# Optimization experiments

Measured on AMD Instinct MI355X. Metric: run time of the kernel, lower is better.

Reference implementation:

```python
import jax, jax.numpy as jnp
import numpy as np

D_MODEL = 2048
N_HEADS = 16
N_KV = 4
D_HEAD = D_MODEL // N_HEADS  # 128
N_REP = N_HEADS // N_KV      # 4
ROPE_BASE = 1000000.0


def _rope_tables(T, d_head, dtype):
    # inv_freq = (1/base)^(2i/d) for i in [0, d/2)
    i = jnp.arange(d_head // 2, dtype=jnp.float32)
    inv_freq = (1.0 / ROPE_BASE) ** (2.0 * i / d_head)
    theta = jnp.arange(T, dtype=jnp.float32)[:, None] * inv_freq[None, :]  # [T, d/2]
    theta = jnp.concatenate([theta, theta], axis=-1)                        # [T, d]
    return jnp.sin(theta).astype(dtype), jnp.cos(theta).astype(dtype)


def _apply_rope(x, sin, cos):
    # x: [B, h, T, d]; sin/cos: [T, d]
    x1, x2 = jnp.split(x, 2, axis=-1)
    rot = jnp.concatenate([-x2, x1], axis=-1)
    return cos[None, None] * x + sin[None, None] * rot


def setup_inputs() -> dict:
    key = jax.random.key(0)
    ks = jax.random.split(key, 9)
    B, T = 2, 2048
    s_in = 1.0 / np.sqrt(D_MODEL)
    return {
        "x": jax.random.normal(ks[0], (B, T, D_MODEL), jnp.float32),
        "wq": jax.random.normal(ks[1], (D_MODEL, N_HEADS * D_HEAD), jnp.float32) * s_in,
        "bq": jax.random.normal(ks[2], (N_HEADS * D_HEAD,), jnp.float32) * 0.02,
        "wk": jax.random.normal(ks[3], (D_MODEL, N_KV * D_HEAD), jnp.float32) * s_in,
        "bk": jax.random.normal(ks[4], (N_KV * D_HEAD,), jnp.float32) * 0.02,
        "wv": jax.random.normal(ks[5], (D_MODEL, N_KV * D_HEAD), jnp.float32) * s_in,
        "bv": jax.random.normal(ks[6], (N_KV * D_HEAD,), jnp.float32) * 0.02,
        "wo": jax.random.normal(ks[7], (D_MODEL, D_MODEL), jnp.float32) * s_in,
    }


def reference(x, wq, bq, wk, bk, wv, bv, wo):
    B, T, C = x.shape
    sin, cos = _rope_tables(T, D_HEAD, x.dtype)

    q = (x @ wq + bq).reshape(B, T, N_HEADS, D_HEAD).transpose(0, 2, 1, 3)  # [B,H,T,d]
    k = (x @ wk + bk).reshape(B, T, N_KV, D_HEAD).transpose(0, 2, 1, 3)     # [B,KV,T,d]
    v = (x @ wv + bv).reshape(B, T, N_KV, D_HEAD).transpose(0, 2, 1, 3)     # [B,KV,T,d]

    q = _apply_rope(q, sin, cos)
    k = _apply_rope(k, sin, cos)

    # GQA: group query heads as [B, KV, rep, T, d] to broadcast against k/v
    qg = q.reshape(B, N_KV, N_REP, T, D_HEAD)
    scale = 1.0 / jnp.sqrt(jnp.asarray(D_HEAD, x.dtype))
    scores = jnp.einsum('bkrqd,bksd->bkrqs', qg, k) * scale  # [B,KV,rep,T,S]

    causal = jnp.tril(jnp.ones((T, T), dtype=bool))
    neg = jnp.asarray(jnp.finfo(x.dtype).min, x.dtype)
    scores = jnp.where(causal[None, None, None], scores, neg)
    p = jax.nn.softmax(scores, axis=-1)

    out = jnp.einsum('bkrqs,bksd->bkrqd', p, v)               # [B,KV,rep,T,d]
    out = out.reshape(B, N_HEADS, T, D_HEAD).transpose(0, 2, 1, 3).reshape(B, T, C)
    return out @ wo, k, v
```

## Files before the change

kernel.cpp:

```cpp
#include <hip/hip_runtime.h>
#include <hip/hip_bf16.h>
#include <math.h>

#define BB 2
#define TT 2048
#define DMODEL 2048
#define NH 16
#define NKV 4
#define DH 128
#define NQKV 3072
#define MM (BB*TT)

typedef unsigned short u16;
typedef unsigned int u32;

typedef __bf16 bf16x8 __attribute__((ext_vector_type(8)));
typedef __bf16 bf16x4 __attribute__((ext_vector_type(4)));
typedef short short4v __attribute__((ext_vector_type(4)));
typedef float f32x4 __attribute__((ext_vector_type(4)));

__device__ __forceinline__ u16 f2b(float f) {
  union { float f; u32 u; } v; v.f = f;
  u32 r = v.u + 0x7fffu + ((v.u >> 16) & 1u);
  return (u16)(r >> 16);
}
__device__ __forceinline__ float b2f(u16 h) {
  union { u32 u; float f; } v; v.u = ((u32)h) << 16;
  return v.f;
}
__device__ __forceinline__ u32 pack2bf(float x, float y) {
  union { float f; u32 u; } a, b; a.f = x; b.f = y;
  return ((a.u + 0x8000u) >> 16) | ((b.u + 0x8000u) & 0xffff0000u);
}

__device__ __forceinline__ void gload16(const void* g, void* l) {
  __builtin_amdgcn_global_load_lds(
      (const __attribute__((address_space(1))) unsigned int*)g,
      (__attribute__((address_space(3))) unsigned int*)l, 16, 0, 0);
}

__device__ __forceinline__ float fast_exp2(float x) {
#if __has_builtin(__builtin_amdgcn_exp2f)
  return __builtin_amdgcn_exp2f(x);
#else
  return __expf(x * 0.6931471805599453f);
#endif
}

__device__ __forceinline__ f32x4 mfma16(bf16x4 a, bf16x4 b, f32x4 c) {
#if __has_builtin(__builtin_amdgcn_mfma_f32_16x16x16bf16_1k)
  union { bf16x4 b; short4v s; } ua, ub;
  ua.b = a; ub.b = b;
  return __builtin_amdgcn_mfma_f32_16x16x16bf16_1k(ua.s, ub.s, c, 0, 0, 0);
#elif __has_builtin(__builtin_amdgcn_mfma_f32_16x16x16_bf16)
  return __builtin_amdgcn_mfma_f32_16x16x16_bf16(a, b, c, 0, 0, 0);
#else
  asm volatile("v_mfma_f32_16x16x16_bf16 %0, %1, %2, %0"
               : "+v"(c) : "v"(a), "v"(b));
  return c;
#endif
}

__global__ void cvt_x_kernel(const float* __restrict__ x, u16* __restrict__ xb, int n4) {
  int i = blockIdx.x * 256 + threadIdx.x;
  if (i < n4) {
    float4 v = ((const float4*)x)[i];
    u32 lo = (u32)f2b(v.x) | ((u32)f2b(v.y) << 16);
    u32 hi = (u32)f2b(v.z) | ((u32)f2b(v.w) << 16);
    uint2 r; r.x = lo; r.y = hi;
    ((uint2*)xb)[i] = r;
  }
}

__global__ void rope_table_kernel(float2* __restrict__ tab) {
  int i = blockIdx.x * 256 + threadIdx.x;
  int t = i >> 6, d = i & 63;
  float inv = exp2f(-(float)d * 0.31143075889569023f);
  float th = (float)t * inv;
  float2 cs; cs.x = cosf(th); cs.y = sinf(th);
  tab[i] = cs;
}

__global__ void transpose_cvt_kernel(const float* __restrict__ src, u16* __restrict__ dst,
                                     int srcCols, int dstRowOff) {
  __shared__ u16 t[64][65];
  int c0 = blockIdx.x * 64, r0 = blockIdx.y * 64;
  int tid = threadIdx.x;
  for (int i = tid; i < 4096; i += 256) {
    int r = i >> 6, c = i & 63;
    t[r][c] = f2b(src[(size_t)(r0 + r) * srcCols + c0 + c]);
  }
  __syncthreads();
  for (int i = tid; i < 4096; i += 256) {
    int n = i >> 6, k = i & 63;
    dst[(size_t)(dstRowOff + c0 + n) * 2048 + r0 + k] = t[k][n];
  }
}


#define BARRIER asm volatile("s_barrier" ::: "memory")
#define LGKM0   asm volatile("s_waitcnt lgkmcnt(0)" ::: "memory")

#define STAGE_A(H, KT, RB) do { \
    const u16* g_ = gA + (size_t)(H) * 262144 + (size_t)(KT) * 64; \
    gload16(g_,          sm + (RB) + tid * 8); \
    gload16(g_ + 131072, sm + (RB) + 4096 + tid * 8); \
  } while (0)

#define STAGE_B(H, KT, RB) do { \
    const u16* g_ = gB + (size_t)(H) * 262144 + (size_t)(KT) * 64; \
    gload16(g_,          sm + (RB) + tid * 8); \
    gload16(g_ + 131072, sm + (RB) + 4096 + tid * 8); \
  } while (0)

#define LDA(BU, MH) do { \
    const u16* ab_ = sm + (BU) + (MH) * 8192 + lra * 64; \
    _Pragma("unroll") \
    for (int mi = 0; mi < 4; mi++) { \
      a[mi][0] = *(const bf16x8*)&ab_[mi * 1024 + as0]; \
      a[mi][1] = *(const bf16x8*)&ab_[mi * 1024 + as1]; \
    } \
  } while (0)

#define LDB(BU, NL) do { \
    const u16* bb_ = sm + (BU) + 16384 + hb * 8192 + lrb * 64; \
    _Pragma("unroll") \
    for (int nj = 0; nj < 2; nj++) { \
      b[(NL)*2+nj][0] = *(const bf16x8*)&bb_[((NL)*2+nj) * 1024 + bs0]; \
      b[(NL)*2+nj][1] = *(const bf16x8*)&bb_[((NL)*2+nj) * 1024 + bs1]; \
    } \
  } while (0)

#define MFMAQ(MH, NL) do { \
    _Pragma("unroll") \
    for (int mi = 0; mi < 4; mi++) \
      _Pragma("unroll") \
      for (int nj = 0; nj < 2; nj++) { \
        acc[(MH)*4+mi][(NL)*2+nj] = __builtin_amdgcn_mfma_f32_16x16x32_bf16( \
            a[mi][0], b[(NL)*2+nj][0], acc[(MH)*4+mi][(NL)*2+nj], 0, 0, 0); \
        acc[(MH)*4+mi][(NL)*2+nj] = __builtin_amdgcn_mfma_f32_16x16x32_bf16( \
            a[mi][1], b[(NL)*2+nj][1], acc[(MH)*4+mi][(NL)*2+nj], 0, 0, 0); \
      } \
  } while (0)

#define TILE4(BU, OBU, KA1, KN) do { \
     \
    LDA(BU, 0); LDB(BU, 0); \
    STAGE_A(1, KA1, (OBU) + 8192); \
    BARRIER; LGKM0; \
    __builtin_amdgcn_s_setprio(1); MFMAQ(0, 0); __builtin_amdgcn_s_setprio(0); \
    BARRIER; \
     \
    LDB(BU, 1); \
    STAGE_A(0, KN, (BU)); \
    BARRIER; LGKM0; \
    __builtin_amdgcn_s_setprio(1); MFMAQ(0, 1); __builtin_amdgcn_s_setprio(0); \
    BARRIER; \
     \
    LDA(BU, 1); \
    STAGE_B(0, KN, (BU) + 16384); \
    BARRIER; LGKM0; \
    __builtin_amdgcn_s_setprio(1); MFMAQ(1, 1); __builtin_amdgcn_s_setprio(0); \
    BARRIER; \
     \
    STAGE_B(1, KN, (BU) + 24576); \
    BARRIER; LGKM0; \
    __builtin_amdgcn_s_setprio(1); MFMAQ(1, 0); __builtin_amdgcn_s_setprio(0); \
    asm volatile("s_waitcnt vmcnt(6)\n\ts_barrier" ::: "memory"); \
  } while (0)

__global__ __launch_bounds__(512, 2) void gemm_qkv_kernel(
    const u16* __restrict__ A, const u16* __restrict__ Bt,
    const float* __restrict__ bq, const float* __restrict__ bk,
    const float* __restrict__ bv, const float2* __restrict__ rtab,
    u16* __restrict__ qb, u16* __restrict__ kb, u16* __restrict__ vt,
    float* __restrict__ outK, float* __restrict__ outV) {
  __shared__ __align__(16) u16 sm[65536];
  const int tid  = threadIdx.x;
  const int lane = tid & 63;
  const int wave = tid >> 6;
  const int wm   = wave >> 2;
  const int wn   = wave & 3;
  const int quad = lane >> 4;
  const int l16  = lane & 15;
  const int m0 = blockIdx.y * 256;
  const int n0 = blockIdx.x * 256;
  const int bx = blockIdx.x;

  const int srow = tid >> 3;
  const int sch  = (tid & 7) ^ (srow & 7);
  const u16* gA = A  + (size_t)(m0 + srow) * 2048 + sch * 8;
  const u16* gB = Bt + (size_t)(n0 + srow) * 2048 + sch * 8;

  const int lra = wm * 64 + l16;
  const int lrb = (wn & 1) * 64 + l16;
  const int hb  = wn >> 1;
  const int as0 = ((quad)     ^ (lra & 7)) << 3;
  const int as1 = ((quad + 4) ^ (lra & 7)) << 3;
  const int bs0 = ((quad)     ^ (lrb & 7)) << 3;
  const int bs1 = ((quad + 4) ^ (lrb & 7)) << 3;

  bf16x8 a[4][2], b[4][2];
  f32x4 acc[8][4];
  const f32x4 zero = {0.f, 0.f, 0.f, 0.f};
#pragma unroll
  for (int i = 0; i < 8; i++)
#pragma unroll
    for (int j = 0; j < 4; j++) acc[i][j] = zero;

  STAGE_A(0, 0, 0);
  STAGE_B(0, 0, 16384);
  STAGE_B(1, 0, 24576);
  STAGE_A(1, 0, 8192);
  STAGE_A(0, 1, 32768);
  STAGE_B(0, 1, 32768 + 16384);
  STAGE_B(1, 1, 32768 + 24576);
  asm volatile("s_waitcnt vmcnt(6)\n\ts_barrier" ::: "memory");

#pragma unroll 1
  for (int it2 = 0; it2 < 16; ++it2) {
    const int ka1 = (2 * it2 + 1) & 31;
    const int kn0 = (2 * it2 + 2) & 31;
    const int kn1 = (2 * it2 + 3) & 31;
    TILE4(0,     32768, ka1, kn0);
    TILE4(32768, 0,     kn0, kn1);
  }

  asm volatile("s_waitcnt vmcnt(0)\n\ts_barrier" ::: "memory");

  const int cls = (bx < 8) ? 0 : ((bx < 10) ? 1 : 2);
#pragma unroll
  for (int nf = 0; nf < 4; nf++) {
    int col = wn * 64 + nf * 16 + l16;
    int gcol = n0 + col;
    float bval = (cls == 0) ? bq[gcol] : ((cls == 1) ? bk[gcol - 2048] : bv[gcol - 2560]);
#pragma unroll
    for (int mh = 0; mh < 2; mh++)
#pragma unroll
      for (int mi = 0; mi < 4; mi++)
#pragma unroll
        for (int r = 0; r < 4; r++) {
          int row = mh * 128 + wm * 64 + mi * 16 + quad * 4 + r;
          int ci = (row * 256 + col) ^ ((row & 7) << 3);
          sm[ci] = f2b(acc[mh * 4 + mi][nf][r] + bval);
        }
  }
  __syncthreads();

  const int bidx = m0 >> 11;
  const int trow0 = m0 & 2047;

  if (cls < 2) {
    const int isQ = (cls == 0);
#pragma unroll
    for (int itq = 0; itq < 8; itq++) {
      int id = tid + itq * 512;
      int lh = id >> 11;
      int rem = id & 2047;
      int row = rem >> 3, oc = rem & 7;
      int t = trow0 + row;
      int rl = t & 63, ttile = t >> 6;
      int sw = (row & 7) << 3;
      int i0 = (row * 256 + lh * 128 + oc * 8);
      uint4 lo = *(const uint4*)&sm[i0 ^ sw];
      uint4 hi = *(const uint4*)&sm[(i0 + 64) ^ sw];
      const u16* plo = (const u16*)&lo;
      const u16* phi = (const u16*)&hi;
      u16 y1[8], y2[8];
      float f1[8], f2v[8];
#pragma unroll
      for (int j = 0; j < 8; j++) {
        float2 cs = rtab[(t << 6) + oc * 8 + j];
        float x1 = b2f(plo[j]), x2 = b2f(phi[j]);
        f1[j]  = cs.x * x1 - cs.y * x2;
        f2v[j] = cs.x * x2 + cs.y * x1;
        y1[j] = f2b(f1[j]);
        y2[j] = f2b(f2v[j]);
      }
      if (isQ) {
        int hh = bx * 2 + lh;
        size_t tb = ((size_t)(bidx * NH + hh) * 32 + ttile) * 8192;
        *(uint4*)&qb[tb + (size_t)((oc)     * 64 + rl) * 8] = *(const uint4*)y1;
        *(uint4*)&qb[tb + (size_t)((oc + 8) * 64 + rl) * 8] = *(const uint4*)y2;
      } else {
        int hh = bx * 2 + lh - 16;
        size_t tb = ((size_t)(bidx * NKV + hh) * 32 + ttile) * 8192;
        *(uint4*)&kb[tb + (size_t)((oc)     * 64 + rl) * 8] = *(const uint4*)y1;
        *(uint4*)&kb[tb + (size_t)((oc + 8) * 64 + rl) * 8] = *(const uint4*)y2;
        size_t base = ((size_t)(bidx * NKV + hh) * TT + t) * DH + oc * 8;
        *(float4*)&outK[base]          = *(const float4*)&f1[0];
        *(float4*)&outK[base + 4]      = *(const float4*)&f1[4];
        *(float4*)&outK[base + 64]     = *(const float4*)&f2v[0];
        *(float4*)&outK[base + 64 + 4] = *(const float4*)&f2v[4];
      }
    }
  } else {
#pragma unroll
    for (int itv = 0; itv < 16; itv++) {
      int id = tid + itv * 512;
      int lh = id >> 12;
      int rem = id & 4095;
      int row = rem >> 4, oc = rem & 15;
      int kvh = bx * 2 + lh - 20;
      int i0 = (row * 256 + lh * 128 + oc * 8) ^ ((row & 7) << 3);
      uint4 v = *(const uint4*)&sm[i0];
      const u16* pv = (const u16*)&v;
      float f[8];
#pragma unroll
      for (int j = 0; j < 8; j++) f[j] = b2f(pv[j]);
      size_t base = ((size_t)(bidx * NKV + kvh) * TT + trow0 + row) * DH + oc * 8;
      *(float4*)&outV[base]     = *(const float4*)&f[0];
      *(float4*)&outV[base + 4] = *(const float4*)&f[4];
    }
#pragma unroll
    for (int itv = 0; itv < 16; itv++) {
      int id = tid + itv * 512;
      int lh = id >> 12;
      int rem = id & 4095;
      int st = rem >> 10;
      int rem2 = rem & 1023;
      int chunk = rem2 >> 7, dl = rem2 & 127;
      int m = chunk >> 2, qd = chunk & 3;
      int kvh = bx * 2 + lh - 20;
      u16 tmp[8];
#pragma unroll
      for (int e = 0; e < 8; e++) {
        int srw = (2 * m + (e >> 2)) * 16 + qd * 4 + (e & 3);
        int row = st * 64 + srw;
        int idx = (row * 256 + lh * 128 + dl) ^ ((row & 7) << 3);
        tmp[e] = sm[idx];
      }
      int tt = (trow0 >> 6) + st;
      size_t tilebase = ((size_t)(bidx * NKV + kvh) * 32 + tt) * 8192;
      *(uint4*)&vt[tilebase + (size_t)(chunk * 128 + dl) * 8] = *(const uint4*)tmp;
    }
  }
}

__global__ __launch_bounds__(256, 3) void gemm_out_kernel(
    const u16* __restrict__ A, const u16* __restrict__ Bt,
    float* __restrict__ Cout, int M, int N, int K) {
  __shared__ __align__(16) u16 smo[16384];
  const int tid  = threadIdx.x;
  const int lane = tid & 63;
  const int wave = tid >> 6;
  const int quad = lane >> 4;
  const int l16  = lane & 15;
  const int m0 = blockIdx.y * 128;
  const int n0 = blockIdx.x * 128;
  const int wrow = (wave >> 1) * 64;
  const int wcol = (wave & 1) * 64;

  f32x4 acc[4][4];
  const f32x4 zero = {0.f, 0.f, 0.f, 0.f};
#pragma unroll
  for (int i = 0; i < 4; i++)
#pragma unroll
    for (int j = 0; j < 4; j++) acc[i][j] = zero;

  const int srow = tid >> 2;
  const int scol = (tid & 3) * 8;
  const u16* ga = A  + (size_t)(m0 + srow) * K + scol;
  const u16* gb = Bt + (size_t)(n0 + srow) * K + scol;

  gload16(ga,                  &smo[tid * 8]);
  gload16(ga + (size_t)64 * K, &smo[2048 + tid * 8]);
  gload16(gb,                  &smo[4096 + tid * 8]);
  gload16(gb + (size_t)64 * K, &smo[6144 + tid * 8]);

  for (int k0 = 0; k0 < K; k0 += 32) {
    const int p = (k0 >> 5) & 1;
    const int kn = (k0 + 32 == K) ? 0 : k0 + 32;
    u16* nb = &smo[(p ^ 1) * 8192];
    gload16(ga + kn,                  nb + tid * 8);
    gload16(ga + kn + (size_t)64 * K, nb + 2048 + tid * 8);
    gload16(gb + kn,                  nb + 4096 + tid * 8);
    gload16(gb + kn + (size_t)64 * K, nb + 6144 + tid * 8);
    asm volatile("s_waitcnt vmcnt(4)\n\ts_barrier" ::: "memory");
    const u16* cb = &smo[p * 8192];
    bf16x8 af[4], bf[4];
#pragma unroll
    for (int mi = 0; mi < 4; mi++)
      af[mi] = *(const bf16x8*)&cb[(wrow + mi * 16 + l16) * 32 + quad * 8];
#pragma unroll
    for (int ni = 0; ni < 4; ni++)
      bf[ni] = *(const bf16x8*)&cb[4096 + (wcol + ni * 16 + l16) * 32 + quad * 8];
    asm volatile("s_waitcnt lgkmcnt(0)\n\ts_barrier" ::: "memory");
#pragma unroll
    for (int mi = 0; mi < 4; mi++)
#pragma unroll
      for (int ni = 0; ni < 4; ni++)
        acc[mi][ni] = __builtin_amdgcn_mfma_f32_16x16x32_bf16(af[mi], bf[ni], acc[mi][ni], 0, 0, 0);
  }
  asm volatile("s_waitcnt vmcnt(0)" ::: "memory");

#pragma unroll
  for (int ni = 0; ni < 4; ni++) {
    int gcol = n0 + wcol + ni * 16 + l16;
#pragma unroll
    for (int mi = 0; mi < 4; mi++) {
#pragma unroll
      for (int r = 0; r < 4; r++) {
        int grow = m0 + wrow + mi * 16 + quad * 4 + r;
        Cout[(size_t)grow * N + gcol] = acc[mi][ni][r];
      }
    }
  }
}

__global__ __launch_bounds__(256, 2) void attn_kernel(
    const u16* __restrict__ Qt, const u16* __restrict__ Kt,
    const u16* __restrict__ Vt, u16* __restrict__ Ob) {
  __shared__ __align__(16) u16 sm[24576];
  u16* vbuf = sm + 16384;

  const int bh = blockIdx.y;
  const int b = bh >> 4, h = bh & 15, kv = h >> 2;
  const int tid = threadIdx.x;
  const int lane = tid & 63;
  const int wave = tid >> 6;
  const int quad = lane >> 4;
  const int l16 = lane & 15;

  const u16* qbase = Qt + (size_t)(b * NH + h) * 32 * 8192;
  const u16* kbase = Kt + (size_t)(b * NKV + kv) * 32 * 8192;
  const u16* vbase = Vt + (size_t)(b * NKV + kv) * 32 * 8192;

  const f32x4 zero = {0.f, 0.f, 0.f, 0.f};
  const float SC2 = 0.08838834764831845f * 1.4426950408889634f;
  const float NEGINF = -__builtin_inff();

  int par = 0;

#pragma unroll
  for (int p = 0; p < 4; p++)
    gload16(kbase + p * 2048 + tid * 8, sm + p * 2048 + tid * 8);

  for (int half = 0; half < 2; ++half) {
    const int qt = half ? (31 - (int)blockIdx.x) : (int)blockIdx.x;
    const int q0 = qt * 64;
    const u16* qtile = qbase + (size_t)qt * 8192;
    const int qrel = wave * 16 + l16;

    bf16x8 qf[4];
#pragma unroll
    for (int kc = 0; kc < 4; kc++)
      qf[kc] = *(const bf16x8*)&qtile[(size_t)((kc * 4 + quad) * 64 + qrel) * 8];

    float mrow = NEGINF, lrow = 0.f;
    f32x4 o[8];
#pragma unroll
    for (int d = 0; d < 8; d++) o[d] = zero;

    for (int kt = 0; kt <= qt; ++kt) {
      u16* kb_c = sm + par * 8192;
      u16* kb_n = sm + (par ^ 1) * 8192;
      const int ktn = (kt < qt) ? kt + 1 : 0;
      const u16* vsrc = vbase + (size_t)kt * 8192;
      const u16* knxt = kbase + (size_t)ktn * 8192;
#pragma unroll
      for (int p = 0; p < 4; p++)
        gload16(vsrc + p * 2048 + tid * 8, vbuf + p * 2048 + tid * 8);
#pragma unroll
      for (int p = 0; p < 4; p++)
        gload16(knxt + p * 2048 + tid * 8, kb_n + p * 2048 + tid * 8);
      asm volatile("s_waitcnt vmcnt(8)\n\ts_barrier" ::: "memory");

      f32x4 sv[4];
#pragma unroll
      for (int mt = 0; mt < 4; mt++) sv[mt] = zero;
#pragma unroll
      for (int kc = 0; kc < 4; kc++) {
#pragma unroll
        for (int mt = 0; mt < 4; mt++) {
          bf16x8 kf = *(const bf16x8*)&kb_c[(size_t)((kc * 4 + quad) * 64 + mt * 16 + l16) * 8];
          sv[mt] = __builtin_amdgcn_mfma_f32_16x16x32_bf16(kf, qf[kc], sv[mt], 0, 0, 0);
        }
      }

      if (kt == qt) {
#pragma unroll
        for (int mt = 0; mt < 4; mt++)
#pragma unroll
          for (int r = 0; r < 4; r++) {
            int srel = mt * 16 + quad * 4 + r;
            if (srel > qrel) sv[mt][r] = NEGINF;
          }
      }
      float mraw = NEGINF;
#pragma unroll
      for (int mt = 0; mt < 4; mt++)
#pragma unroll
        for (int r = 0; r < 4; r++) mraw = fmaxf(mraw, sv[mt][r]);
      mraw = fmaxf(mraw, __shfl_xor(mraw, 16));
      mraw = fmaxf(mraw, __shfl_xor(mraw, 32));

      float mnew = fmaxf(mrow, mraw);
      float alpha = fast_exp2((mrow - mnew) * SC2);
      mrow = mnew;
      float msc = mnew * SC2;
      float lsum = 0.f;
#pragma unroll
      for (int mt = 0; mt < 4; mt++) {
#pragma unroll
        for (int r = 0; r < 4; r++) {
          float p = fast_exp2(__builtin_fmaf(sv[mt][r], SC2, -msc));
          sv[mt][r] = p;
          lsum += p;
        }
      }
      lrow = lrow * alpha + lsum;
      bf16x4 pb[4];
#pragma unroll
      for (int mt = 0; mt < 4; mt++) {
        union { u32 u[2]; bf16x4 v; } pu;
        pu.u[0] = pack2bf(sv[mt][0], sv[mt][1]);
        pu.u[1] = pack2bf(sv[mt][2], sv[mt][3]);
        pb[mt] = pu.v;
      }
#pragma unroll
      for (int dt = 0; dt < 8; dt++) {
        o[dt][0] *= alpha; o[dt][1] *= alpha; o[dt][2] *= alpha; o[dt][3] *= alpha;
      }

      asm volatile("s_waitcnt vmcnt(4)\n\ts_barrier" ::: "memory");
#pragma unroll
      for (int m = 0; m < 2; m++) {
#pragma unroll
        for (int dt = 0; dt < 8; dt++) {
          bf16x8 vf = *(const bf16x8*)&vbuf[(size_t)(((m * 4 + quad) * 128) + dt * 16 + l16) * 8];
          bf16x4 vlo = __builtin_shufflevector(vf, vf, 0, 1, 2, 3);
          bf16x4 vhi = __builtin_shufflevector(vf, vf, 4, 5, 6, 7);
          o[dt] = mfma16(vlo, pb[2 * m],     o[dt]);
          o[dt] = mfma16(vhi, pb[2 * m + 1], o[dt]);
        }
      }
      asm volatile("s_barrier" ::: "memory");
      par ^= 1;
    }

    lrow += __shfl_xor(lrow, 16);
    lrow += __shfl_xor(lrow, 32);
    float inv = 1.0f / lrow;
    int t = q0 + qrel;
    size_t rowbase = (size_t)(b * TT + t) * DMODEL + h * DH;
#pragma unroll
    for (int dt = 0; dt < 8; dt++) {
      uint2 w;
      w.x = pack2bf(o[dt][0] * inv, o[dt][1] * inv);
      w.y = pack2bf(o[dt][2] * inv, o[dt][3] * inv);
      *(uint2*)&Ob[rowbase + dt * 16 + quad * 4] = w;
    }
  }
  asm volatile("s_waitcnt vmcnt(0)" ::: "memory");
}

extern "C" void kernel_launch(void* const* d_in, const int* in_sizes, int n_in,
                              void* d_out, int out_size, void* d_ws, size_t ws_size,
                              hipStream_t stream) {
  (void)in_sizes; (void)n_in; (void)out_size; (void)ws_size;
  const float* x  = (const float*)d_in[0];
  const float* wq = (const float*)d_in[1];
  const float* bq = (const float*)d_in[2];
  const float* wk = (const float*)d_in[3];
  const float* bk = (const float*)d_in[4];
  const float* wv = (const float*)d_in[5];
  const float* bv = (const float*)d_in[6];
  const float* wo = (const float*)d_in[7];
  float* out = (float*)d_out;

  char* ws = (char*)d_ws;
  u16*    xb    = (u16*)(ws);
  u16*    wqkvT = (u16*)(ws + 16777216);
  u16*    woT   = (u16*)(ws + 29360128);
  float2* rtab  = (float2*)(ws + 37748736);
  u16*    qb    = (u16*)(ws + 38797312);
  u16*    kb    = (u16*)(ws + 55574528);
  u16*    vt    = (u16*)(ws + 59768832);
  u16*    ob    = (u16*)(ws + 63963136);

  float* outK = out + (size_t)BB * TT * DMODEL;
  float* outV = outK + (size_t)BB * NKV * TT * DH;

  cvt_x_kernel<<<8192, 256, 0, stream>>>(x, xb, (BB * TT * DMODEL) / 4);
  rope_table_kernel<<<512, 256, 0, stream>>>(rtab);
  transpose_cvt_kernel<<<dim3(32, 32), 256, 0, stream>>>(wq, wqkvT, 2048, 0);
  transpose_cvt_kernel<<<dim3(8, 32),  256, 0, stream>>>(wk, wqkvT, 512, 2048);
  transpose_cvt_kernel<<<dim3(8, 32),  256, 0, stream>>>(wv, wqkvT, 512, 2560);
  transpose_cvt_kernel<<<dim3(32, 32), 256, 0, stream>>>(wo, woT, 2048, 0);

  gemm_qkv_kernel<<<dim3(NQKV / 256, MM / 256), 512, 0, stream>>>(
      xb, wqkvT, bq, bk, bv, rtab, qb, kb, vt, outK, outV);

  attn_kernel<<<dim3(16, BB * NH), 256, 0, stream>>>(qb, kb, vt, ob);

  gemm_out_kernel<<<dim3(DMODEL / 128, MM / 128), 256, 0, stream>>>(
      ob, woT, out, MM, DMODEL, DMODEL);
}
```

Measured before the change: 303.3 us.

## Process paired causal query tiles together in attention; merge weight transposes

The attention kernel now processes both query tiles of a causal pair (p and 31-p) in one pass over K/V. It streams each K/V tile once and reuses it for both tiles, instead of running two sequential passes that each reload K/V. It also adds lazy softmax rescaling, which skips the alpha rescale when the new row max exceeds the old one by no more than a threshold, and adds MFMA priority hints. The four weight transpose launches are fused into one launch, and extra lgkmcnt waits are inserted in the QKV GEMM pipeline. Holding two sets of accumulators raises register pressure.

```diff
diff --git a/kernel.cpp b/kernel.cpp
--- a/kernel.cpp
+++ b/kernel.cpp
@@ -81,10 +81,20 @@
   tab[i] = cs;
 }
 
-__global__ void transpose_cvt_kernel(const float* __restrict__ src, u16* __restrict__ dst,
-                                     int srcCols, int dstRowOff) {
+__global__ void transpose_cvt_all_kernel(const float* __restrict__ wq,
+                                         const float* __restrict__ wk,
+                                         const float* __restrict__ wv,
+                                         const float* __restrict__ wo,
+                                         u16* __restrict__ wqkvT,
+                                         u16* __restrict__ woT) {
   __shared__ u16 t[64][65];
-  int c0 = blockIdx.x * 64, r0 = blockIdx.y * 64;
+  int bx = blockIdx.x;
+  const float* src; u16* dst; int srcCols, rowOff, cb;
+  if (bx < 32)      { src = wq; dst = wqkvT; srcCols = 2048; rowOff = 0;    cb = bx; }
+  else if (bx < 40) { src = wk; dst = wqkvT; srcCols = 512;  rowOff = 2048; cb = bx - 32; }
+  else if (bx < 48) { src = wv; dst = wqkvT; srcCols = 512;  rowOff = 2560; cb = bx - 40; }
+  else              { src = wo; dst = woT;   srcCols = 2048; rowOff = 0;    cb = bx - 48; }
+  int c0 = cb * 64, r0 = blockIdx.y * 64;
   int tid = threadIdx.x;
   for (int i = tid; i < 4096; i += 256) {
     int r = i >> 6, c = i & 63;
@@ -93,7 +103,7 @@
   __syncthreads();
   for (int i = tid; i < 4096; i += 256) {
     int n = i >> 6, k = i & 63;
-    dst[(size_t)(dstRowOff + c0 + n) * 2048 + r0 + k] = t[k][n];
+    dst[(size_t)(rowOff + c0 + n) * 2048 + r0 + k] = t[k][n];
   }
 }
 
@@ -147,6 +157,7 @@
      \
     LDA(BU, 0); LDB(BU, 0); \
     STAGE_A(1, KA1, (OBU) + 8192); \
+    asm volatile("s_waitcnt lgkmcnt(8)" ::: "memory"); \
     BARRIER; LGKM0; \
     __builtin_amdgcn_s_setprio(1); MFMAQ(0, 0); __builtin_amdgcn_s_setprio(0); \
     BARRIER; \
@@ -159,6 +170,7 @@
      \
     LDA(BU, 1); \
     STAGE_B(0, KN, (BU) + 16384); \
+    asm volatile("s_waitcnt lgkmcnt(4)" ::: "memory"); \
     BARRIER; LGKM0; \
     __builtin_amdgcn_s_setprio(1); MFMAQ(1, 1); __builtin_amdgcn_s_setprio(0); \
     BARRIER; \
@@ -408,6 +420,58 @@
   }
 }
 
+
+#define SM_STRIP(sv, mrow, lrow, pb, o, qt_) do { \
+    if (kt == (qt_)) { \
+      _Pragma("unroll") \
+      for (int mt = 0; mt < 4; mt++) { \
+        _Pragma("unroll") \
+        for (int r = 0; r < 4; r++) { \
+          int srel = mt * 16 + quad * 4 + r; \
+          if (srel > qrel) sv[mt][r] = NEGINF; \
+        } \
+      } \
+    } \
+    float mraw = NEGINF; \
+    _Pragma("unroll") \
+    for (int mt = 0; mt < 4; mt++) { \
+      _Pragma("unroll") \
+      for (int r = 0; r < 4; r++) mraw = fmaxf(mraw, sv[mt][r]); \
+    } \
+    mraw = fmaxf(mraw, __shfl_xor(mraw, 16)); \
+    mraw = fmaxf(mraw, __shfl_xor(mraw, 32)); \
+    bool noresc = __all(mraw <= mrow + 8.0f);    \
+    float mnew = noresc ? mrow : fmaxf(mrow, mraw); \
+    float msc = mnew * SC2; \
+    float lsum = 0.f; \
+    _Pragma("unroll") \
+    for (int mt = 0; mt < 4; mt++) { \
+      _Pragma("unroll") \
+      for (int r = 0; r < 4; r++) { \
+        float pe = fast_exp2(__builtin_fmaf(sv[mt][r], SC2, -msc)); \
+        sv[mt][r] = pe; lsum += pe; \
+      } \
+    } \
+    if (noresc) { \
+      lrow += lsum; \
+    } else { \
+      float alpha = fast_exp2((mrow - mnew) * SC2); \
+      mrow = mnew; \
+      lrow = lrow * alpha + lsum; \
+      _Pragma("unroll") \
+      for (int dt = 0; dt < 8; dt++) { \
+        o[dt][0] *= alpha; o[dt][1] *= alpha; o[dt][2] *= alpha; o[dt][3] *= alpha; \
+      } \
+    } \
+    _Pragma("unroll") \
+    for (int mt = 0; mt < 4; mt++) { \
+      union { u32 u[2]; bf16x4 v; } pu_; \
+      pu_.u[0] = pack2bf(sv[mt][0], sv[mt][1]); \
+      pu_.u[1] = pack2bf(sv[mt][2], sv[mt][3]); \
+      pb[mt] = pu_.v; \
+    } \
+  } while (0)
+
 __global__ __launch_bounds__(256, 2) void attn_kernel(
     const u16* __restrict__ Qt, const u16* __restrict__ Kt,
     const u16* __restrict__ Vt, u16* __restrict__ Ob) {
@@ -430,100 +494,80 @@
   const float SC2 = 0.08838834764831845f * 1.4426950408889634f;
   const float NEGINF = -__builtin_inff();
 
+  const int p = (bh & 16) ? (15 - (int)blockIdx.x) : (int)blockIdx.x;
+  const int qtA = p, qtB = 31 - p;
+  const int qrel = wave * 16 + l16;
+
   int par = 0;
-
-#pragma unroll
-  for (int p = 0; p < 4; p++)
-    gload16(kbase + p * 2048 + tid * 8, sm + p * 2048 + tid * 8);
-
-  for (int half = 0; half < 2; ++half) {
-    const int qt = half ? (31 - (int)blockIdx.x) : (int)blockIdx.x;
-    const int q0 = qt * 64;
-    const u16* qtile = qbase + (size_t)qt * 8192;
-    const int qrel = wave * 16 + l16;
-
-    bf16x8 qf[4];
-#pragma unroll
-    for (int kc = 0; kc < 4; kc++)
-      qf[kc] = *(const bf16x8*)&qtile[(size_t)((kc * 4 + quad) * 64 + qrel) * 8];
-
-    float mrow = NEGINF, lrow = 0.f;
-    f32x4 o[8];
-#pragma unroll
-    for (int d = 0; d < 8; d++) o[d] = zero;
-
-    for (int kt = 0; kt <= qt; ++kt) {
-      u16* kb_c = sm + par * 8192;
-      u16* kb_n = sm + (par ^ 1) * 8192;
-      const int ktn = (kt < qt) ? kt + 1 : 0;
-      const u16* vsrc = vbase + (size_t)kt * 8192;
-      const u16* knxt = kbase + (size_t)ktn * 8192;
-#pragma unroll
-      for (int p = 0; p < 4; p++)
-        gload16(vsrc + p * 2048 + tid * 8, vbuf + p * 2048 + tid * 8);
-#pragma unroll
-      for (int p = 0; p < 4; p++)
-        gload16(knxt + p * 2048 + tid * 8, kb_n + p * 2048 + tid * 8);
-      asm volatile("s_waitcnt vmcnt(8)\n\ts_barrier" ::: "memory");
-
-      f32x4 sv[4];
-#pragma unroll
-      for (int mt = 0; mt < 4; mt++) sv[mt] = zero;
+#pragma unroll
+  for (int pp = 0; pp < 4; pp++)
+    gload16(kbase + pp * 2048 + tid * 8, sm + pp * 2048 + tid * 8);
+
+  const u16* qpA = qbase + (size_t)qtA * 8192;
+  const u16* qpB = qbase + (size_t)qtB * 8192;
+  bf16x8 qfA[4], qfB[4];
+#pragma unroll
+  for (int kc = 0; kc < 4; kc++) {
+    qfA[kc] = *(const bf16x8*)&qpA[(size_t)((kc * 4 + quad) * 64 + qrel) * 8];
+    qfB[kc] = *(const bf16x8*)&qpB[(size_t)((kc * 4 + quad) * 64 + qrel) * 8];
+  }
+
+  float mA = NEGINF, lA = 0.f, mB = NEGINF, lB = 0.f;
+  f32x4 oA[8], oB[8];
+#pragma unroll
+  for (int d = 0; d < 8; d++) { oA[d] = zero; oB[d] = zero; }
+
+  for (int kt = 0; kt <= qtB; ++kt) {
+    u16* kb_c = sm + par * 8192;
+    u16* kb_n = sm + (par ^ 1) * 8192;
+    const int ktn = (kt < qtB) ? kt + 1 : 0;
+    const u16* vsrc = vbase + (size_t)kt * 8192;
+    const u16* knxt = kbase + (size_t)ktn * 8192;
+#pragma unroll
+    for (int pp = 0; pp < 4; pp++)
+      gload16(vsrc + pp * 2048 + tid * 8, vbuf + pp * 2048 + tid * 8);
+#pragma unroll
+    for (int pp = 0; pp < 4; pp++)
+      gload16(knxt + pp * 2048 + tid * 8, kb_n + pp * 2048 + tid * 8);
+    asm volatile("s_waitcnt vmcnt(8)\n\ts_barrier" ::: "memory");
+
+    const bool actA = (kt <= qtA);
+    f32x4 svA[4], svB[4];
+#pragma unroll
+    for (int mt = 0; mt < 4; mt++) { svA[mt] = zero; svB[mt] = zero; }
+
+    if (actA) {
+      __builtin_amdgcn_s_setprio(1);
 #pragma unroll
       for (int kc = 0; kc < 4; kc++) {
 #pragma unroll
         for (int mt = 0; mt < 4; mt++) {
           bf16x8 kf = *(const bf16x8*)&kb_c[(size_t)((kc * 4 + quad) * 64 + mt * 16 + l16) * 8];
-          sv[mt] = __builtin_amdgcn_mfma_f32_16x16x32_bf16(kf, qf[kc], sv[mt], 0, 0, 0);
+          svB[mt] = __builtin_amdgcn_mfma_f32_16x16x32_bf16(kf, qfB[kc], svB[mt], 0, 0, 0);
+          svA[mt] = __builtin_amdgcn_mfma_f32_16x16x32_bf16(kf, qfA[kc], svA[mt], 0, 0, 0);
         }
       }
-
-      if (kt == qt) {
-#pragma unroll
-        for (int mt = 0; mt < 4; mt++)
-#pragma unroll
-          for (int r = 0; r < 4; r++) {
-            int srel = mt * 16 + quad * 4 + r;
-            if (srel > qrel) sv[mt][r] = NEGINF;
-          }
-      }
-      float mraw = NEGINF;
-#pragma unroll
-      for (int mt = 0; mt < 4; mt++)
-#pragma unroll
-        for (int r = 0; r < 4; r++) mraw = fmaxf(mraw, sv[mt][r]);
-      mraw = fmaxf(mraw, __shfl_xor(mraw, 16));
-      mraw = fmaxf(mraw, __shfl_xor(mraw, 32));
-
-      float mnew = fmaxf(mrow, mraw);
-      float alpha = fast_exp2((mrow - mnew) * SC2);
-      mrow = mnew;
-      float msc = mnew * SC2;
-      float lsum = 0.f;
-#pragma unroll
-      for (int mt = 0; mt < 4; mt++) {
-#pragma unroll
-        for (int r = 0; r < 4; r++) {
-          float p = fast_exp2(__builtin_fmaf(sv[mt][r], SC2, -msc));
-          sv[mt][r] = p;
-          lsum += p;
+      __builtin_amdgcn_s_setprio(0);
+    } else {
+      __builtin_amdgcn_s_setprio(1);
+#pragma unroll
+      for (int kc = 0; kc < 4; kc++) {
+#pragma unroll
+        for (int mt = 0; mt < 4; mt++) {
+          bf16x8 kf = *(const bf16x8*)&kb_c[(size_t)((kc * 4 + quad) * 64 + mt * 16 + l16) * 8];
+          svB[mt] = __builtin_amdgcn_mfma_f32_16x16x32_bf16(kf, qfB[kc], svB[mt], 0, 0, 0);
         }
       }
-      lrow = lrow * alpha + lsum;
-      bf16x4 pb[4];
-#pragma unroll
-      for (int mt = 0; mt < 4; mt++) {
-        union { u32 u[2]; bf16x4 v; } pu;
-        pu.u[0] = pack2bf(sv[mt][0], sv[mt][1]);
-        pu.u[1] = pack2bf(sv[mt][2], sv[mt][3]);
-        pb[mt] = pu.v;
-      }
-#pragma unroll
-      for (int dt = 0; dt < 8; dt++) {
-        o[dt][0] *= alpha; o[dt][1] *= alpha; o[dt][2] *= alpha; o[dt][3] *= alpha;
-      }
-
-      asm volatile("s_waitcnt vmcnt(4)\n\ts_barrier" ::: "memory");
+      __builtin_amdgcn_s_setprio(0);
+    }
+
+    bf16x4 pbA[4], pbB[4];
+    SM_STRIP(svB, mB, lB, pbB, oB, qtB);
+    if (actA) SM_STRIP(svA, mA, lA, pbA, oA, qtA);
+
+    asm volatile("s_waitcnt vmcnt(4)\n\ts_barrier" ::: "memory");
+    if (actA) {
+      __builtin_amdgcn_s_setprio(1);
 #pragma unroll
       for (int m = 0; m < 2; m++) {
 #pragma unroll
@@ -531,24 +575,57 @@
           bf16x8 vf = *(const bf16x8*)&vbuf[(size_t)(((m * 4 + quad) * 128) + dt * 16 + l16) * 8];
           bf16x4 vlo = __builtin_shufflevector(vf, vf, 0, 1, 2, 3);
           bf16x4 vhi = __builtin_shufflevector(vf, vf, 4, 5, 6, 7);
-          o[dt] = mfma16(vlo, pb[2 * m],     o[dt]);
-          o[dt] = mfma16(vhi, pb[2 * m + 1], o[dt]);
+          oB[dt] = mfma16(vlo, pbB[2 * m],     oB[dt]);
+          oB[dt] = mfma16(vhi, pbB[2 * m + 1], oB[dt]);
+          oA[dt] = mfma16(vlo, pbA[2 * m],     oA[dt]);
+          oA[dt] = mfma16(vhi, pbA[2 * m + 1], oA[dt]);
         }
       }
-      asm volatile("s_barrier" ::: "memory");
-      par ^= 1;
-    }
-
-    lrow += __shfl_xor(lrow, 16);
-    lrow += __shfl_xor(lrow, 32);
-    float inv = 1.0f / lrow;
-    int t = q0 + qrel;
+      __builtin_amdgcn_s_setprio(0);
+    } else {
+      __builtin_amdgcn_s_setprio(1);
+#pragma unroll
+      for (int m = 0; m < 2; m++) {
+#pragma unroll
+        for (int dt = 0; dt < 8; dt++) {
+          bf16x8 vf = *(const bf16x8*)&vbuf[(size_t)(((m * 4 + quad) * 128) + dt * 16 + l16) * 8];
+          bf16x4 vlo = __builtin_shufflevector(vf, vf, 0, 1, 2, 3);
+          bf16x4 vhi = __builtin_shufflevector(vf, vf, 4, 5, 6, 7);
+          oB[dt] = mfma16(vlo, pbB[2 * m],     oB[dt]);
+          oB[dt] = mfma16(vhi, pbB[2 * m + 1], oB[dt]);
+        }
+      }
+      __builtin_amdgcn_s_setprio(0);
+    }
+    asm volatile("s_barrier" ::: "memory");
+    par ^= 1;
+  }
+
+  {
+    lA += __shfl_xor(lA, 16);
+    lA += __shfl_xor(lA, 32);
+    float inv = 1.0f / lA;
+    int t = qtA * 64 + qrel;
     size_t rowbase = (size_t)(b * TT + t) * DMODEL + h * DH;
 #pragma unroll
     for (int dt = 0; dt < 8; dt++) {
       uint2 w;
-      w.x = pack2bf(o[dt][0] * inv, o[dt][1] * inv);
-      w.y = pack2bf(o[dt][2] * inv, o[dt][3] * inv);
+      w.x = pack2bf(oA[dt][0] * inv, oA[dt][1] * inv);
+      w.y = pack2bf(oA[dt][2] * inv, oA[dt][3] * inv);
+      *(uint2*)&Ob[rowbase + dt * 16 + quad * 4] = w;
+    }
+  }
+  {
+    lB += __shfl_xor(lB, 16);
+    lB += __shfl_xor(lB, 32);
+    float inv = 1.0f / lB;
+    int t = qtB * 64 + qrel;
+    size_t rowbase = (size_t)(b * TT + t) * DMODEL + h * DH;
+#pragma unroll
+    for (int dt = 0; dt < 8; dt++) {
+      uint2 w;
+      w.x = pack2bf(oB[dt][0] * inv, oB[dt][1] * inv);
+      w.y = pack2bf(oB[dt][2] * inv, oB[dt][3] * inv);
       *(uint2*)&Ob[rowbase + dt * 16 + quad * 4] = w;
     }
   }
@@ -584,10 +661,7 @@
 
   cvt_x_kernel<<<8192, 256, 0, stream>>>(x, xb, (BB * TT * DMODEL) / 4);
   rope_table_kernel<<<512, 256, 0, stream>>>(rtab);
-  transpose_cvt_kernel<<<dim3(32, 32), 256, 0, stream>>>(wq, wqkvT, 2048, 0);
-  transpose_cvt_kernel<<<dim3(8, 32),  256, 0, stream>>>(wk, wqkvT, 512, 2048);
-  transpose_cvt_kernel<<<dim3(8, 32),  256, 0, stream>>>(wv, wqkvT, 512, 2560);
-  transpose_cvt_kernel<<<dim3(32, 32), 256, 0, stream>>>(wo, woT, 2048, 0);
+  transpose_cvt_all_kernel<<<dim3(80, 32), 256, 0, stream>>>(wq, wk, wv, wo, wqkvT, woT);
 
   gemm_qkv_kernel<<<dim3(NQKV / 256, MM / 256), 512, 0, stream>>>(
       xb, wqkvT, bq, bk, bv, rtab, qb, kb, vt, outK, outV);
```

Result: no change. 307.0 us (+1.2%).

## Merge weight transposes, split attention blocks per tile, add lazy softmax rescale

Applied to the files above, without the earlier changes.

The four weight transpose launches are merged into a single kernel launch that picks its source tensor from the block index. The attention kernel now gives each q-tile its own block (32 per head, interleaved so short and long tiles alternate) instead of pairing two tiles per block. It also skips the online-softmax rescale unless the new max exceeds the old by more than a threshold, and raises wave priority around the MFMA sections. The QKV GEMM gains partial lgkmcnt waits before its barriers. The threshold-based lazy rescale keeps exact normalization but lets unnormalized exponents grow, up to about 2^(8*scale), which is a small overflow and precision risk.

```diff
diff --git a/kernel.cpp b/kernel.cpp
--- a/kernel.cpp
+++ b/kernel.cpp
@@ -81,10 +81,20 @@
   tab[i] = cs;
 }
 
-__global__ void transpose_cvt_kernel(const float* __restrict__ src, u16* __restrict__ dst,
-                                     int srcCols, int dstRowOff) {
+__global__ void transpose_cvt_all_kernel(const float* __restrict__ wq,
+                                         const float* __restrict__ wk,
+                                         const float* __restrict__ wv,
+                                         const float* __restrict__ wo,
+                                         u16* __restrict__ wqkvT,
+                                         u16* __restrict__ woT) {
   __shared__ u16 t[64][65];
-  int c0 = blockIdx.x * 64, r0 = blockIdx.y * 64;
+  int bx = blockIdx.x;
+  const float* src; u16* dst; int srcCols, rowOff, cb;
+  if (bx < 32)      { src = wq; dst = wqkvT; srcCols = 2048; rowOff = 0;    cb = bx; }
+  else if (bx < 40) { src = wk; dst = wqkvT; srcCols = 512;  rowOff = 2048; cb = bx - 32; }
+  else if (bx < 48) { src = wv; dst = wqkvT; srcCols = 512;  rowOff = 2560; cb = bx - 40; }
+  else              { src = wo; dst = woT;   srcCols = 2048; rowOff = 0;    cb = bx - 48; }
+  int c0 = cb * 64, r0 = blockIdx.y * 64;
   int tid = threadIdx.x;
   for (int i = tid; i < 4096; i += 256) {
     int r = i >> 6, c = i & 63;
@@ -93,7 +103,7 @@
   __syncthreads();
   for (int i = tid; i < 4096; i += 256) {
     int n = i >> 6, k = i & 63;
-    dst[(size_t)(dstRowOff + c0 + n) * 2048 + r0 + k] = t[k][n];
+    dst[(size_t)(rowOff + c0 + n) * 2048 + r0 + k] = t[k][n];
   }
 }
 
@@ -147,6 +157,7 @@
      \
     LDA(BU, 0); LDB(BU, 0); \
     STAGE_A(1, KA1, (OBU) + 8192); \
+    asm volatile("s_waitcnt lgkmcnt(8)" ::: "memory"); \
     BARRIER; LGKM0; \
     __builtin_amdgcn_s_setprio(1); MFMAQ(0, 0); __builtin_amdgcn_s_setprio(0); \
     BARRIER; \
@@ -159,6 +170,7 @@
      \
     LDA(BU, 1); \
     STAGE_B(0, KN, (BU) + 16384); \
+    asm volatile("s_waitcnt lgkmcnt(4)" ::: "memory"); \
     BARRIER; LGKM0; \
     __builtin_amdgcn_s_setprio(1); MFMAQ(1, 1); __builtin_amdgcn_s_setprio(0); \
     BARRIER; \
@@ -430,127 +442,134 @@
   const float SC2 = 0.08838834764831845f * 1.4426950408889634f;
   const float NEGINF = -__builtin_inff();
 
+  const int x = blockIdx.x;
+  const int qt = (x & 1) ? (31 - (x >> 1)) : (x >> 1);
+  const int q0 = qt * 64;
+  const int qrel = wave * 16 + l16;
+
   int par = 0;
-
-#pragma unroll
-  for (int p = 0; p < 4; p++)
-    gload16(kbase + p * 2048 + tid * 8, sm + p * 2048 + tid * 8);
-
-  for (int half = 0; half < 2; ++half) {
-    const int qt = half ? (31 - (int)blockIdx.x) : (int)blockIdx.x;
-    const int q0 = qt * 64;
-    const u16* qtile = qbase + (size_t)qt * 8192;
-    const int qrel = wave * 16 + l16;
-
-    bf16x8 qf[4];
-#pragma unroll
-    for (int kc = 0; kc < 4; kc++)
-      qf[kc] = *(const bf16x8*)&qtile[(size_t)((kc * 4 + quad) * 64 + qrel) * 8];
-
-    float mrow = NEGINF, lrow = 0.f;
-    f32x4 o[8];
-#pragma unroll
-    for (int d = 0; d < 8; d++) o[d] = zero;
-
-    for (int kt = 0; kt <= qt; ++kt) {
-      u16* kb_c = sm + par * 8192;
-      u16* kb_n = sm + (par ^ 1) * 8192;
-      const int ktn = (kt < qt) ? kt + 1 : 0;
-      const u16* vsrc = vbase + (size_t)kt * 8192;
-      const u16* knxt = kbase + (size_t)ktn * 8192;
-#pragma unroll
-      for (int p = 0; p < 4; p++)
-        gload16(vsrc + p * 2048 + tid * 8, vbuf + p * 2048 + tid * 8);
-#pragma unroll
-      for (int p = 0; p < 4; p++)
-        gload16(knxt + p * 2048 + tid * 8, kb_n + p * 2048 + tid * 8);
-      asm volatile("s_waitcnt vmcnt(8)\n\ts_barrier" ::: "memory");
-
-      f32x4 sv[4];
-#pragma unroll
-      for (int mt = 0; mt < 4; mt++) sv[mt] = zero;
-#pragma unroll
-      for (int kc = 0; kc < 4; kc++) {
-#pragma unroll
-        for (int mt = 0; mt < 4; mt++) {
-          bf16x8 kf = *(const bf16x8*)&kb_c[(size_t)((kc * 4 + quad) * 64 + mt * 16 + l16) * 8];
-          sv[mt] = __builtin_amdgcn_mfma_f32_16x16x32_bf16(kf, qf[kc], sv[mt], 0, 0, 0);
+#pragma unroll
+  for (int pp = 0; pp < 4; pp++)
+    gload16(kbase + pp * 2048 + tid * 8, sm + pp * 2048 + tid * 8);
+
+  const u16* qtile = qbase + (size_t)qt * 8192;
+  bf16x8 qf[4];
+#pragma unroll
+  for (int kc = 0; kc < 4; kc++)
+    qf[kc] = *(const bf16x8*)&qtile[(size_t)((kc * 4 + quad) * 64 + qrel) * 8];
+
+  float mrow = NEGINF, lrow = 0.f;
+  f32x4 o[8];
+#pragma unroll
+  for (int d = 0; d < 8; d++) o[d] = zero;
+
+  for (int kt = 0; kt <= qt; ++kt) {
+    u16* kb_c = sm + par * 8192;
+    u16* kb_n = sm + (par ^ 1) * 8192;
+    const int ktn = (kt < qt) ? kt + 1 : 0;
+    const u16* vsrc = vbase + (size_t)kt * 8192;
+    const u16* knxt = kbase + (size_t)ktn * 8192;
+#pragma unroll
+    for (int pp = 0; pp < 4; pp++)
+      gload16(vsrc + pp * 2048 + tid * 8, vbuf + pp * 2048 + tid * 8);
+#pragma unroll
+    for (int pp = 0; pp < 4; pp++)
+      gload16(knxt + pp * 2048 + tid * 8, kb_n + pp * 2048 + tid * 8);
+    asm volatile("s_waitcnt vmcnt(8)\n\ts_barrier" ::: "memory");
+
+    f32x4 sv[4];
+#pragma unroll
+    for (int mt = 0; mt < 4; mt++) sv[mt] = zero;
+    __builtin_amdgcn_s_setprio(1);
+#pragma unroll
+    for (int kc = 0; kc < 4; kc++) {
+#pragma unroll
+      for (int mt = 0; mt < 4; mt++) {
+        bf16x8 kf = *(const bf16x8*)&kb_c[(size_t)((kc * 4 + quad) * 64 + mt * 16 + l16) * 8];
+        sv[mt] = __builtin_amdgcn_mfma_f32_16x16x32_bf16(kf, qf[kc], sv[mt], 0, 0, 0);
+      }
+    }
+    __builtin_amdgcn_s_setprio(0);
+
+    if (kt == qt) {
+#pragma unroll
+      for (int mt = 0; mt < 4; mt++)
+#pragma unroll
+        for (int r = 0; r < 4; r++) {
+          int srel = mt * 16 + quad * 4 + r;
+          if (srel > qrel) sv[mt][r] = NEGINF;
         }
-      }
-
-      if (kt == qt) {
-#pragma unroll
-        for (int mt = 0; mt < 4; mt++)
-#pragma unroll
-          for (int r = 0; r < 4; r++) {
-            int srel = mt * 16 + quad * 4 + r;
-            if (srel > qrel) sv[mt][r] = NEGINF;
-          }
-      }
-      float mraw = NEGINF;
-#pragma unroll
-      for (int mt = 0; mt < 4; mt++)
-#pragma unroll
-        for (int r = 0; r < 4; r++) mraw = fmaxf(mraw, sv[mt][r]);
-      mraw = fmaxf(mraw, __shfl_xor(mraw, 16));
-      mraw = fmaxf(mraw, __shfl_xor(mraw, 32));
-
-      float mnew = fmaxf(mrow, mraw);
+    }
+    float mraw = NEGINF;
+#pragma unroll
+    for (int mt = 0; mt < 4; mt++)
+#pragma unroll
+      for (int r = 0; r < 4; r++) mraw = fmaxf(mraw, sv[mt][r]);
+    mraw = fmaxf(mraw, __shfl_xor(mraw, 16));
+    mraw = fmaxf(mraw, __shfl_xor(mraw, 32));
+
+    bool noresc = __all(mraw <= mrow + 8.0f);
+    float mnew = noresc ? mrow : fmaxf(mrow, mraw);
+    float msc = mnew * SC2;
+    float lsum = 0.f;
+#pragma unroll
+    for (int mt = 0; mt < 4; mt++) {
+#pragma unroll
+      for (int r = 0; r < 4; r++) {
+        float pe = fast_exp2(__builtin_fmaf(sv[mt][r], SC2, -msc));
+        sv[mt][r] = pe;
+        lsum += pe;
+      }
+    }
+    if (noresc) {
+      lrow += lsum;
+    } else {
       float alpha = fast_exp2((mrow - mnew) * SC2);
       mrow = mnew;
-      float msc = mnew * SC2;
-      float lsum = 0.f;
-#pragma unroll
-      for (int mt = 0; mt < 4; mt++) {
-#pragma unroll
-        for (int r = 0; r < 4; r++) {
-          float p = fast_exp2(__builtin_fmaf(sv[mt][r], SC2, -msc));
-          sv[mt][r] = p;
-          lsum += p;
-        }
-      }
       lrow = lrow * alpha + lsum;
-      bf16x4 pb[4];
-#pragma unroll
-      for (int mt = 0; mt < 4; mt++) {
-        union { u32 u[2]; bf16x4 v; } pu;
-        pu.u[0] = pack2bf(sv[mt][0], sv[mt][1]);
-        pu.u[1] = pack2bf(sv[mt][2], sv[mt][3]);
-        pb[mt] = pu.v;
-      }
 #pragma unroll
       for (int dt = 0; dt < 8; dt++) {
         o[dt][0] *= alpha; o[dt][1] *= alpha; o[dt][2] *= alpha; o[dt][3] *= alpha;
       }
-
-      asm volatile("s_waitcnt vmcnt(4)\n\ts_barrier" ::: "memory");
-#pragma unroll
-      for (int m = 0; m < 2; m++) {
-#pragma unroll
-        for (int dt = 0; dt < 8; dt++) {
-          bf16x8 vf = *(const bf16x8*)&vbuf[(size_t)(((m * 4 + quad) * 128) + dt * 16 + l16) * 8];
-          bf16x4 vlo = __builtin_shufflevector(vf, vf, 0, 1, 2, 3);
-          bf16x4 vhi = __builtin_shufflevector(vf, vf, 4, 5, 6, 7);
-          o[dt] = mfma16(vlo, pb[2 * m],     o[dt]);
-          o[dt] = mfma16(vhi, pb[2 * m + 1], o[dt]);
-        }
-      }
-      asm volatile("s_barrier" ::: "memory");
-      par ^= 1;
-    }
-
-    lrow += __shfl_xor(lrow, 16);
-    lrow += __shfl_xor(lrow, 32);
-    float inv = 1.0f / lrow;
-    int t = q0 + qrel;
-    size_t rowbase = (size_t)(b * TT + t) * DMODEL + h * DH;
-#pragma unroll
-    for (int dt = 0; dt < 8; dt++) {
-      uint2 w;
-      w.x = pack2bf(o[dt][0] * inv, o[dt][1] * inv);
-      w.y = pack2bf(o[dt][2] * inv, o[dt][3] * inv);
-      *(uint2*)&Ob[rowbase + dt * 16 + quad * 4] = w;
-    }
+    }
+    bf16x4 pb[4];
+#pragma unroll
+    for (int mt = 0; mt < 4; mt++) {
+      union { u32 u[2]; bf16x4 v; } pu;
+      pu.u[0] = pack2bf(sv[mt][0], sv[mt][1]);
+      pu.u[1] = pack2bf(sv[mt][2], sv[mt][3]);
+      pb[mt] = pu.v;
+    }
+
+    asm volatile("s_waitcnt vmcnt(4)\n\ts_barrier" ::: "memory");
+    __builtin_amdgcn_s_setprio(1);
+#pragma unroll
+    for (int m = 0; m < 2; m++) {
+#pragma unroll
+      for (int dt = 0; dt < 8; dt++) {
+        bf16x8 vf = *(const bf16x8*)&vbuf[(size_t)(((m * 4 + quad) * 128) + dt * 16 + l16) * 8];
+        bf16x4 vlo = __builtin_shufflevector(vf, vf, 0, 1, 2, 3);
+        bf16x4 vhi = __builtin_shufflevector(vf, vf, 4, 5, 6, 7);
+        o[dt] = mfma16(vlo, pb[2 * m],     o[dt]);
+        o[dt] = mfma16(vhi, pb[2 * m + 1], o[dt]);
+      }
+    }
+    __builtin_amdgcn_s_setprio(0);
+    asm volatile("s_barrier" ::: "memory");
+    par ^= 1;
+  }
+
+  lrow += __shfl_xor(lrow, 16);
+  lrow += __shfl_xor(lrow, 32);
+  float inv = 1.0f / lrow;
+  int t = q0 + qrel;
+  size_t rowbase = (size_t)(b * TT + t) * DMODEL + h * DH;
+#pragma unroll
+  for (int dt = 0; dt < 8; dt++) {
+    uint2 w;
+    w.x = pack2bf(o[dt][0] * inv, o[dt][1] * inv);
+    w.y = pack2bf(o[dt][2] * inv, o[dt][3] * inv);
+    *(uint2*)&Ob[rowbase + dt * 16 + quad * 4] = w;
   }
   asm volatile("s_waitcnt vmcnt(0)" ::: "memory");
 }
@@ -584,15 +603,12 @@
 
   cvt_x_kernel<<<8192, 256, 0, stream>>>(x, xb, (BB * TT * DMODEL) / 4);
   rope_table_kernel<<<512, 256, 0, stream>>>(rtab);
-  transpose_cvt_kernel<<<dim3(32, 32), 256, 0, stream>>>(wq, wqkvT, 2048, 0);
-  transpose_cvt_kernel<<<dim3(8, 32),  256, 0, stream>>>(wk, wqkvT, 512, 2048);
-  transpose_cvt_kernel<<<dim3(8, 32),  256, 0, stream>>>(wv, wqkvT, 512, 2560);
-  transpose_cvt_kernel<<<dim3(32, 32), 256, 0, stream>>>(wo, woT, 2048, 0);
+  transpose_cvt_all_kernel<<<dim3(80, 32), 256, 0, stream>>>(wq, wk, wv, wo, wqkvT, woT);
 
   gemm_qkv_kernel<<<dim3(NQKV / 256, MM / 256), 512, 0, stream>>>(
       xb, wqkvT, bq, bk, bv, rtab, qb, kb, vt, outK, outV);
 
-  attn_kernel<<<dim3(16, BB * NH), 256, 0, stream>>>(qb, kb, vt, ob);
+  attn_kernel<<<dim3(32, BB * NH), 256, 0, stream>>>(qb, kb, vt, ob);
 
   gemm_out_kernel<<<dim3(DMODEL / 128, MM / 128), 256, 0, stream>>>(
       ob, woT, out, MM, DMODEL, DMODEL);
```

New measurement: 330.3 us. 8.9% more time.
